# Performance work log

Measured on AMD Instinct MI355X. Metric: run time of the kernel, lower is better.

## Reference

```python
import jax, jax.numpy as jnp
import numpy as np

N_NODES = 100000


def _gcn_layer(h, W, b, src, dst, norm, n):
    # h: [N, Fin] -> transform then normalized scatter-add aggregation
    h = h @ W                                   # [N, Fout]
    msg = h[src] * norm[:, None]                # [E', Fout] gather + scale
    out = jax.ops.segment_sum(msg, dst, num_segments=n)  # scatter-add
    return out + b


def setup_inputs() -> dict:
    key = jax.random.key(0)
    k1, k2, k3, k4 = jax.random.split(key, 4)
    N, F_IN, HID, C, E = N_NODES, 512, 128, 40, 1600000
    x = jax.random.normal(k1, (N, F_IN), dtype=jnp.float32)
    edge_index = jax.random.randint(k2, (2, E), 0, N, dtype=jnp.int64)
    W1 = jax.random.normal(k3, (F_IN, HID), dtype=jnp.float32) * (1.0 / np.sqrt(F_IN))
    b1 = jnp.zeros((HID,), dtype=jnp.float32)
    W2 = jax.random.normal(k4, (HID, C), dtype=jnp.float32) * (1.0 / np.sqrt(HID))
    b2 = jnp.zeros((C,), dtype=jnp.float32)
    return {"x": x, "edge_index": edge_index, "W1": W1, "b1": b1, "W2": W2, "b2": b2}


def reference(x, edge_index, W1, b1, W2, b2):
    n = x.shape[0]
    # add self-loops (GCNConv default)
    loop = jnp.arange(n, dtype=edge_index.dtype)
    src = jnp.concatenate([edge_index[0], loop])
    dst = jnp.concatenate([edge_index[1], loop])
    # symmetric normalization: deg counted on destination (in-degree, incl. self-loop)
    deg = jax.ops.segment_sum(jnp.ones_like(dst, dtype=x.dtype), dst, num_segments=n)
    dis = jnp.where(deg > 0, jax.lax.rsqrt(deg), 0.0)  # deg^{-1/2}
    norm = dis[src] * dis[dst]                          # per-edge weight

    h = jax.nn.relu(_gcn_layer(x, W1, b1, src, dst, norm, n))
    # dropout: identity in eval mode (training=False)
    h = _gcn_layer(h, W2, b2, src, dst, norm, n)
    return jax.nn.log_softmax(h, axis=1)
```

## Files before the change

### kernel.cpp

```cpp
#include <hip/hip_runtime.h>
#include <hip/hip_bf16.h>


#define F_IN 512
#define HID  128
#define NC   40

typedef __attribute__((ext_vector_type(8))) short bf16x8;
typedef __attribute__((ext_vector_type(4))) float f32x4v;

__device__ __forceinline__ ushort f2bf(float f) {
    union { float f; unsigned u; } x; x.f = f;
    unsigned r = x.u + 0x7FFFu + ((x.u >> 16) & 1u);
    return (ushort)(r >> 16);
}
__device__ __forceinline__ float bf2f(ushort u) {
    return __uint_as_float((unsigned)u << 16);
}

__global__ void count_deg(const int* __restrict__ dst, int E, unsigned* __restrict__ cnt) {
    int t = blockIdx.x * blockDim.x + threadIdx.x;
    if (t < E) atomicAdd(&cnt[dst[t]], 1u);
}

__global__ void dis_k(const unsigned* __restrict__ cnt, float* __restrict__ dis, int N) {
    int t = blockIdx.x * blockDim.x + threadIdx.x;
    if (t < N) dis[t] = rsqrtf((float)cnt[t] + 1.0f);
}

__global__ __launch_bounds__(1024) void scan_block(const unsigned* __restrict__ cnt,
                                                   unsigned* __restrict__ offs,
                                                   unsigned* __restrict__ bsums, int N) {
    __shared__ unsigned s[1024];
    int tid = threadIdx.x;
    int i = blockIdx.x * 1024 + tid;
    unsigned v = (i < N) ? cnt[i] + 1u : 0u;
    s[tid] = v;
    __syncthreads();
    #pragma unroll
    for (int d = 1; d < 1024; d <<= 1) {
        unsigned t = (tid >= d) ? s[tid - d] : 0u;
        __syncthreads();
        s[tid] += t;
        __syncthreads();
    }
    if (i < N) offs[i] = s[tid] - v;
    if (tid == 1023) bsums[blockIdx.x] = s[1023];
}

__global__ __launch_bounds__(1024) void scan_bsums(unsigned* __restrict__ bsums, int nb) {
    __shared__ unsigned s[1024];
    int tid = threadIdx.x;
    unsigned v = (tid < nb) ? bsums[tid] : 0u;
    s[tid] = v;
    __syncthreads();
    #pragma unroll
    for (int d = 1; d < 1024; d <<= 1) {
        unsigned t = (tid >= d) ? s[tid - d] : 0u;
        __syncthreads();
        s[tid] += t;
        __syncthreads();
    }
    if (tid < nb) bsums[tid] = s[tid] - v;
}

__global__ __launch_bounds__(1024) void scan_add(unsigned* __restrict__ offs,
                                                 const unsigned* __restrict__ bsums,
                                                 int N, unsigned total) {
    int i = blockIdx.x * 1024 + threadIdx.x;
    if (i < N) offs[i] += bsums[blockIdx.x];
    if (i == 0) offs[N] = total;
}

__global__ void fill_csr(const int* __restrict__ src, const int* __restrict__ dst,
                         const unsigned* __restrict__ offs, unsigned* __restrict__ cursor,
                         int* __restrict__ col, int E, int N) {
    int t = blockIdx.x * blockDim.x + threadIdx.x;
    if (t >= E + N) return;
    int s, d;
    if (t < E) { s = src[t]; d = dst[t]; } else { s = d = t - E; }
    unsigned pos = offs[d] + atomicAdd(&cursor[d], 1u);
    col[pos] = s;
}

__global__ void w1pack(const float* __restrict__ W1, ushort* __restrict__ Bp) {
    int t = blockIdx.x * 256 + threadIdx.x;
    int j = t & 7, n = (t >> 3) & 127, kb = (t >> 10) & 3, s = t >> 12;
    int k = s * 32 + kb * 8 + j;
    Bp[t] = f2bf(W1[(size_t)k * HID + n]);
}

__global__ void w2pack(const float* __restrict__ W2, ushort* __restrict__ Bp) {
    int t = blockIdx.x * 256 + threadIdx.x;
    int j = t & 7;
    int i2 = t >> 3;
    int n = i2 % 48;
    int i3 = i2 / 48;
    int kb = i3 & 3, ks = i3 >> 2;
    int k = ks * 32 + kb * 8 + j;
    float v = (n < NC) ? W2[(size_t)k * NC + n] : 0.f;
    Bp[t] = f2bf(v);
}

__global__ __launch_bounds__(256) void gemm1_mfma(const float* __restrict__ A,
                                                  const ushort* __restrict__ Bp,
                                                  const float* __restrict__ dis,
                                                  ushort* __restrict__ C, int N) {
    __shared__ __align__(16) ushort As[128 * 40];
    __shared__ __align__(16) ushort Bs[4096];
    const int tid  = threadIdx.x;
    const int wave = tid >> 6;
    const int lane = tid & 63;
    const int quad = lane >> 4;
    const int mr   = lane & 15;
    const int bm   = blockIdx.x * 128;

    const int r  = tid >> 1;
    const int hh = tid & 1;
    const bool arow_ok = (bm + r) < N;
    const float* arow = A + (size_t)(bm + r) * F_IN + hh * 16;

    f32x4v acc[2][8];
    #pragma unroll
    for (int i = 0; i < 2; i++)
        #pragma unroll
        for (int t = 0; t < 8; t++)
            acc[i][t] = (f32x4v){0.f, 0.f, 0.f, 0.f};

    for (int s = 0; s < 16; s++) {
        {
            const uint4* srcp = (const uint4*)(Bp + (size_t)s * 4096) + tid * 2;
            uint4 v0 = srcp[0], v1 = srcp[1];
            uint4* dstp = (uint4*)Bs + tid * 2;
            dstp[0] = v0; dstp[1] = v1;
        }
        {
            ushort tmp[16];
            if (arow_ok) {
                const float4* ap = (const float4*)(arow + s * 32);
                #pragma unroll
                for (int i = 0; i < 4; i++) {
                    float4 v = ap[i];
                    tmp[i*4+0] = f2bf(v.x); tmp[i*4+1] = f2bf(v.y);
                    tmp[i*4+2] = f2bf(v.z); tmp[i*4+3] = f2bf(v.w);
                }
            } else {
                #pragma unroll
                for (int i = 0; i < 16; i++) tmp[i] = 0;
            }
            uint4* dstp = (uint4*)&As[r * 40 + hh * 16];
            dstp[0] = ((const uint4*)tmp)[0];
            dstp[1] = ((const uint4*)tmp)[1];
        }
        __syncthreads();
        bf16x8 a0 = *(const bf16x8*)&As[(wave * 32 + mr) * 40 + quad * 8];
        bf16x8 a1 = *(const bf16x8*)&As[(wave * 32 + 16 + mr) * 40 + quad * 8];
        #pragma unroll
        for (int t = 0; t < 8; t++) {
            bf16x8 b = *(const bf16x8*)&Bs[quad * 1024 + (t * 16 + mr) * 8];
            acc[0][t] = __builtin_amdgcn_mfma_f32_16x16x32_bf16(a0, b, acc[0][t], 0, 0, 0);
            acc[1][t] = __builtin_amdgcn_mfma_f32_16x16x32_bf16(a1, b, acc[1][t], 0, 0, 0);
        }
        __syncthreads();
    }
    #pragma unroll
    for (int i = 0; i < 2; i++) {
        int row0 = bm + wave * 32 + i * 16 + quad * 4;
        #pragma unroll
        for (int rr = 0; rr < 4; rr++) {
            int row = row0 + rr;
            if (row < N) {
                float ds = dis[row];
                #pragma unroll
                for (int t = 0; t < 8; t++)
                    C[(size_t)row * HID + t * 16 + mr] = f2bf(acc[i][t][rr] * ds);
            }
        }
    }
}

__global__ __launch_bounds__(256) void agg1_k(const ushort* __restrict__ h,
                                              const int* __restrict__ col,
                                              const unsigned* __restrict__ offs,
                                              const float* __restrict__ dis,
                                              ushort* __restrict__ out, int N) {
    int node = blockIdx.x * 8 + (threadIdx.x >> 5);
    if (node >= N) return;
    int lane = threadIdx.x & 31;
    unsigned p0 = offs[node], p1 = offs[node + 1];
    float4 a0 = make_float4(0.f, 0.f, 0.f, 0.f);
    float4 a1 = make_float4(0.f, 0.f, 0.f, 0.f);
    float4 a2 = make_float4(0.f, 0.f, 0.f, 0.f);
    float4 a3 = make_float4(0.f, 0.f, 0.f, 0.f);
    unsigned p = p0;
    for (; p + 4 <= p1; p += 4) {
        int s0 = col[p], s1 = col[p+1], s2 = col[p+2], s3 = col[p+3];
        ushort4 v0 = *(const ushort4*)(h + (size_t)s0 * HID + lane * 4);
        ushort4 v1 = *(const ushort4*)(h + (size_t)s1 * HID + lane * 4);
        ushort4 v2 = *(const ushort4*)(h + (size_t)s2 * HID + lane * 4);
        ushort4 v3 = *(const ushort4*)(h + (size_t)s3 * HID + lane * 4);
        a0.x += bf2f(v0.x); a0.y += bf2f(v0.y); a0.z += bf2f(v0.z); a0.w += bf2f(v0.w);
        a1.x += bf2f(v1.x); a1.y += bf2f(v1.y); a1.z += bf2f(v1.z); a1.w += bf2f(v1.w);
        a2.x += bf2f(v2.x); a2.y += bf2f(v2.y); a2.z += bf2f(v2.z); a2.w += bf2f(v2.w);
        a3.x += bf2f(v3.x); a3.y += bf2f(v3.y); a3.z += bf2f(v3.z); a3.w += bf2f(v3.w);
    }
    for (; p < p1; ++p) {
        int s = col[p];
        ushort4 v = *(const ushort4*)(h + (size_t)s * HID + lane * 4);
        a0.x += bf2f(v.x); a0.y += bf2f(v.y); a0.z += bf2f(v.z); a0.w += bf2f(v.w);
    }
    float dd = dis[node];
    float4 a;
    a.x = ((a0.x + a1.x) + (a2.x + a3.x)) * dd;
    a.y = ((a0.y + a1.y) + (a2.y + a3.y)) * dd;
    a.z = ((a0.z + a1.z) + (a2.z + a3.z)) * dd;
    a.w = ((a0.w + a1.w) + (a2.w + a3.w)) * dd;
    ushort4 o;
    o.x = f2bf(a.x); o.y = f2bf(a.y); o.z = f2bf(a.z); o.w = f2bf(a.w);
    *(ushort4*)(out + (size_t)node * HID + lane * 4) = o;
}

__global__ __launch_bounds__(256) void gemm2_mfma(const ushort* __restrict__ A,
                                                  const float* __restrict__ b1,
                                                  const ushort* __restrict__ W2p,
                                                  const float* __restrict__ dis,
                                                  ushort* __restrict__ h2, int N) {
    __shared__ __align__(16) ushort As[128 * 136];
    __shared__ __align__(16) ushort Bs[6144];
    const int tid = threadIdx.x;
    const int bm = blockIdx.x * 128;

    {
        const uint4* s4 = (const uint4*)W2p;
        uint4* d4 = (uint4*)Bs;
        #pragma unroll
        for (int i = 0; i < 3; i++) d4[tid + i * 256] = s4[tid + i * 256];
    }
    {
        const int r  = tid >> 1;
        const int hh = tid & 1;
        const int row = bm + r;
        const float* brow = b1 + hh * 64;
        if (row < N) {
            const ushort* arow = A + (size_t)row * HID + hh * 64;
            #pragma unroll
            for (int i = 0; i < 8; i++) {
                uint4 raw = *(const uint4*)(arow + i * 8);
                const ushort* u = (const ushort*)&raw;
                ushort tmp[8];
                #pragma unroll
                for (int j = 0; j < 8; j++)
                    tmp[j] = f2bf(fmaxf(bf2f(u[j]) + brow[i * 8 + j], 0.f));
                *(uint4*)&As[r * 136 + hh * 64 + i * 8] = *(const uint4*)tmp;
            }
        } else {
            #pragma unroll
            for (int i = 0; i < 8; i++) {
                uint4 z = {0, 0, 0, 0};
                *(uint4*)&As[r * 136 + hh * 64 + i * 8] = z;
            }
        }
    }
    __syncthreads();

    const int wave = tid >> 6;
    const int lane = tid & 63;
    const int quad = lane >> 4;
    const int mr   = lane & 15;
    f32x4v acc[2][3];
    #pragma unroll
    for (int i = 0; i < 2; i++)
        #pragma unroll
        for (int t = 0; t < 3; t++)
            acc[i][t] = (f32x4v){0.f, 0.f, 0.f, 0.f};
    #pragma unroll
    for (int ks = 0; ks < 4; ks++) {
        bf16x8 a0 = *(const bf16x8*)&As[(wave * 32 + mr) * 136 + ks * 32 + quad * 8];
        bf16x8 a1 = *(const bf16x8*)&As[(wave * 32 + 16 + mr) * 136 + ks * 32 + quad * 8];
        #pragma unroll
        for (int t = 0; t < 3; t++) {
            bf16x8 b = *(const bf16x8*)&Bs[((ks * 4 + quad) * 48 + t * 16 + mr) * 8];
            acc[0][t] = __builtin_amdgcn_mfma_f32_16x16x32_bf16(a0, b, acc[0][t], 0, 0, 0);
            acc[1][t] = __builtin_amdgcn_mfma_f32_16x16x32_bf16(a1, b, acc[1][t], 0, 0, 0);
        }
    }
    #pragma unroll
    for (int i = 0; i < 2; i++) {
        #pragma unroll
        for (int rr = 0; rr < 4; rr++) {
            int node = bm + wave * 32 + i * 16 + quad * 4 + rr;
            if (node < N) {
                float ds = dis[node];
                #pragma unroll
                for (int t = 0; t < 3; t++) {
                    int c = t * 16 + mr;
                    if (c < NC)
                        h2[(size_t)node * NC + c] = f2bf(acc[i][t][rr] * ds);
                }
            }
        }
    }
}

__global__ __launch_bounds__(256) void agg2_ls(const ushort* __restrict__ h2,
                                               const int* __restrict__ col,
                                               const unsigned* __restrict__ offs,
                                               const float* __restrict__ dis,
                                               const float* __restrict__ b2,
                                               float* __restrict__ out, int N) {
    int node = blockIdx.x * 32 + (threadIdx.x >> 3);
    if (node >= N) return;
    int lane = threadIdx.x & 7;
    unsigned p0 = offs[node], p1 = offs[node + 1];
    float4 a  = make_float4(0.f, 0.f, 0.f, 0.f);
    float4 a2 = make_float4(0.f, 0.f, 0.f, 0.f);
    float4 c  = make_float4(0.f, 0.f, 0.f, 0.f);
    float4 c2 = make_float4(0.f, 0.f, 0.f, 0.f);
    unsigned p = p0;
    for (; p + 2 <= p1; p += 2) {
        int s0 = col[p], s1 = col[p + 1];
        const ushort* hp0 = h2 + (size_t)s0 * NC;
        const ushort* hp1 = h2 + (size_t)s1 * NC;
        ushort4 v0 = *(const ushort4*)(hp0 + lane * 4);
        ushort4 v1 = *(const ushort4*)(hp1 + lane * 4);
        a.x += bf2f(v0.x); a.y += bf2f(v0.y); a.z += bf2f(v0.z); a.w += bf2f(v0.w);
        c.x += bf2f(v1.x); c.y += bf2f(v1.y); c.z += bf2f(v1.z); c.w += bf2f(v1.w);
        if (lane < 2) {
            ushort4 w0 = *(const ushort4*)(hp0 + 32 + lane * 4);
            ushort4 w1 = *(const ushort4*)(hp1 + 32 + lane * 4);
            a2.x += bf2f(w0.x); a2.y += bf2f(w0.y); a2.z += bf2f(w0.z); a2.w += bf2f(w0.w);
            c2.x += bf2f(w1.x); c2.y += bf2f(w1.y); c2.z += bf2f(w1.z); c2.w += bf2f(w1.w);
        }
    }
    for (; p < p1; ++p) {
        int s = col[p];
        const ushort* hp = h2 + (size_t)s * NC;
        ushort4 v = *(const ushort4*)(hp + lane * 4);
        a.x += bf2f(v.x); a.y += bf2f(v.y); a.z += bf2f(v.z); a.w += bf2f(v.w);
        if (lane < 2) {
            ushort4 w = *(const ushort4*)(hp + 32 + lane * 4);
            a2.x += bf2f(w.x); a2.y += bf2f(w.y); a2.z += bf2f(w.z); a2.w += bf2f(w.w);
        }
    }
    float dd = dis[node];
    float4 bb = *(const float4*)(b2 + lane * 4);
    a.x = (a.x + c.x) * dd + bb.x; a.y = (a.y + c.y) * dd + bb.y;
    a.z = (a.z + c.z) * dd + bb.z; a.w = (a.w + c.w) * dd + bb.w;
    if (lane < 2) {
        float4 b2v = *(const float4*)(b2 + 32 + lane * 4);
        a2.x = (a2.x + c2.x) * dd + b2v.x; a2.y = (a2.y + c2.y) * dd + b2v.y;
        a2.z = (a2.z + c2.z) * dd + b2v.z; a2.w = (a2.w + c2.w) * dd + b2v.w;
    }
    float m = fmaxf(fmaxf(a.x, a.y), fmaxf(a.z, a.w));
    if (lane < 2) m = fmaxf(m, fmaxf(fmaxf(a2.x, a2.y), fmaxf(a2.z, a2.w)));
    #pragma unroll
    for (int d = 1; d < 8; d <<= 1) m = fmaxf(m, __shfl_xor(m, d, 8));
    float s = __expf(a.x - m) + __expf(a.y - m) + __expf(a.z - m) + __expf(a.w - m);
    if (lane < 2) s += __expf(a2.x - m) + __expf(a2.y - m) + __expf(a2.z - m) + __expf(a2.w - m);
    #pragma unroll
    for (int d = 1; d < 8; d <<= 1) s += __shfl_xor(s, d, 8);
    float lse = m + __logf(s);
    float* op = out + (size_t)node * NC;
    *(float4*)(op + lane * 4) = make_float4(a.x - lse, a.y - lse, a.z - lse, a.w - lse);
    if (lane < 2)
        *(float4*)(op + 32 + lane * 4) = make_float4(a2.x - lse, a2.y - lse, a2.z - lse, a2.w - lse);
}

extern "C" void kernel_launch(void* const* d_in, const int* in_sizes, int n_in,
                              void* d_out, int out_size, void* d_ws, size_t ws_size,
                              hipStream_t stream) {
    const float* x  = (const float*)d_in[0];
    const int*   ei = (const int*)d_in[1];
    const float* W1 = (const float*)d_in[2];
    const float* b1 = (const float*)d_in[3];
    const float* W2 = (const float*)d_in[4];
    const float* b2 = (const float*)d_in[5];
    float* out = (float*)d_out;

    const int N = in_sizes[0] / F_IN;
    const int E = in_sizes[1] / 2;
    const int EN = E + N;
    const int* src = ei;
    const int* dst = ei + E;

    char* ws = (char*)d_ws;
    size_t o = 0;
    unsigned* cnt  = (unsigned*)(ws + o); o += (size_t)N * 4;
    float*    dis  = (float*)   (ws + o); o += (size_t)N * 4;
    unsigned* offs = (unsigned*)(ws + o); o += (size_t)(N + 4) * 4;
    unsigned* bsums= (unsigned*)(ws + o); o += 4096;
    int*      col  = (int*)     (ws + o); o += (size_t)EN * 4;
    o = (o + 15) & ~(size_t)15;
    ushort*   W1p  = (ushort*)  (ws + o); o += (size_t)F_IN * HID * 2;
    o = (o + 15) & ~(size_t)15;
    ushort*   W2p  = (ushort*)  (ws + o); o += 6144 * 2;
    o = (o + 15) & ~(size_t)15;
    ushort*   h1   = (ushort*)  (ws + o); o += (size_t)N * HID * 2;
    o = (o + 15) & ~(size_t)15;
    ushort*   ag1  = (ushort*)  (ws + o); o += (size_t)N * HID * 2;
    o = (o + 15) & ~(size_t)15;
    ushort*   h2   = (ushort*)  (ws + o); o += (size_t)N * NC * 2;

    const int nb = (N + 1023) / 1024;

    hipMemsetAsync(cnt, 0, (size_t)N * 4, stream);
    count_deg<<<(E + 255) / 256, 256, 0, stream>>>(dst, E, cnt);
    dis_k<<<(N + 255) / 256, 256, 0, stream>>>(cnt, dis, N);

    scan_block<<<nb, 1024, 0, stream>>>(cnt, offs, bsums, N);
    scan_bsums<<<1, 1024, 0, stream>>>(bsums, nb);
    scan_add<<<nb, 1024, 0, stream>>>(offs, bsums, N, (unsigned)EN);

    hipMemsetAsync(cnt, 0, (size_t)N * 4, stream);
    fill_csr<<<(EN + 255) / 256, 256, 0, stream>>>(src, dst, offs, cnt, col, E, N);

    w1pack<<<(F_IN * HID) / 256, 256, 0, stream>>>(W1, W1p);
    w2pack<<<6144 / 256, 256, 0, stream>>>(W2, W2p);

    gemm1_mfma<<<(N + 127) / 128, 256, 0, stream>>>(x, W1p, dis, h1, N);
    agg1_k<<<(N + 7) / 8, 256, 0, stream>>>(h1, col, offs, dis, ag1, N);

    gemm2_mfma<<<(N + 127) / 128, 256, 0, stream>>>(ag1, b1, W2p, dis, h2, N);
    agg2_ls<<<(N + 31) / 32, 256, 0, stream>>>(h2, col, offs, dis, b2, out, N);
}
```

Measured before the change: 618.6 us.

## Fuse setup kernels, drop self-loop CSR entries, double-buffer gemm1, widen aggregation loads

Moves the deg^-1/2 computation into the scan kernel and merges the two weight-pack kernels into one launch. Self-loops are no longer stored in the CSR; each aggregation instead reads the node's own row directly, which shrinks the edge list and drops the second memset. gemm1 now loads A fragments straight from global memory into registers and double-buffers the B tile in shared memory, removing the A staging through shared memory. Both aggregation kernels switch to 16-byte loads per lane, with fewer lanes per node and idle lanes in agg2 for the 40-class case.

```diff
diff --git a/kernel.cpp b/kernel.cpp
--- a/kernel.cpp
+++ b/kernel.cpp
@@ -23,18 +23,15 @@
     if (t < E) atomicAdd(&cnt[dst[t]], 1u);
 }
 
-__global__ void dis_k(const unsigned* __restrict__ cnt, float* __restrict__ dis, int N) {
-    int t = blockIdx.x * blockDim.x + threadIdx.x;
-    if (t < N) dis[t] = rsqrtf((float)cnt[t] + 1.0f);
-}
-
 __global__ __launch_bounds__(1024) void scan_block(const unsigned* __restrict__ cnt,
                                                    unsigned* __restrict__ offs,
-                                                   unsigned* __restrict__ bsums, int N) {
+                                                   unsigned* __restrict__ bsums,
+                                                   float* __restrict__ dis, int N) {
     __shared__ unsigned s[1024];
     int tid = threadIdx.x;
     int i = blockIdx.x * 1024 + tid;
-    unsigned v = (i < N) ? cnt[i] + 1u : 0u;
+    unsigned v = (i < N) ? cnt[i] : 0u;
+    if (i < N) dis[i] = rsqrtf((float)v + 1.0f);
     s[tid] = v;
     __syncthreads();
     #pragma unroll
@@ -74,40 +71,41 @@
 
 __global__ void fill_csr(const int* __restrict__ src, const int* __restrict__ dst,
                          const unsigned* __restrict__ offs, unsigned* __restrict__ cursor,
-                         int* __restrict__ col, int E, int N) {
+                         int* __restrict__ col, int E) {
     int t = blockIdx.x * blockDim.x + threadIdx.x;
-    if (t >= E + N) return;
-    int s, d;
-    if (t < E) { s = src[t]; d = dst[t]; } else { s = d = t - E; }
+    if (t >= E) return;
+    int s = src[t], d = dst[t];
     unsigned pos = offs[d] + atomicAdd(&cursor[d], 1u);
     col[pos] = s;
 }
 
-__global__ void w1pack(const float* __restrict__ W1, ushort* __restrict__ Bp) {
+__global__ void packW(const float* __restrict__ W1, const float* __restrict__ W2,
+                      ushort* __restrict__ W1p, ushort* __restrict__ W2p) {
     int t = blockIdx.x * 256 + threadIdx.x;
-    int j = t & 7, n = (t >> 3) & 127, kb = (t >> 10) & 3, s = t >> 12;
-    int k = s * 32 + kb * 8 + j;
-    Bp[t] = f2bf(W1[(size_t)k * HID + n]);
-}
-
-__global__ void w2pack(const float* __restrict__ W2, ushort* __restrict__ Bp) {
-    int t = blockIdx.x * 256 + threadIdx.x;
-    int j = t & 7;
-    int i2 = t >> 3;
-    int n = i2 % 48;
-    int i3 = i2 / 48;
-    int kb = i3 & 3, ks = i3 >> 2;
-    int k = ks * 32 + kb * 8 + j;
-    float v = (n < NC) ? W2[(size_t)k * NC + n] : 0.f;
-    Bp[t] = f2bf(v);
+    if (t < 65536) {
+        int j = t & 7, n = (t >> 3) & 127, kb = (t >> 10) & 3, s = t >> 12;
+        int k = s * 32 + kb * 8 + j;
+        W1p[t] = f2bf(W1[(size_t)k * HID + n]);
+    } else {
+        int q = t - 65536;
+        if (q < 6144) {
+            int j = q & 7;
+            int i2 = q >> 3;
+            int n = i2 % 48;
+            int i3 = i2 / 48;
+            int kb = i3 & 3, ks = i3 >> 2;
+            int k = ks * 32 + kb * 8 + j;
+            float v = (n < NC) ? W2[(size_t)k * NC + n] : 0.f;
+            W2p[q] = f2bf(v);
+        }
+    }
 }
 
 __global__ __launch_bounds__(256) void gemm1_mfma(const float* __restrict__ A,
                                                   const ushort* __restrict__ Bp,
                                                   const float* __restrict__ dis,
                                                   ushort* __restrict__ C, int N) {
-    __shared__ __align__(16) ushort As[128 * 40];
-    __shared__ __align__(16) ushort Bs[4096];
+    __shared__ __align__(16) ushort Bs[2][4096];
     const int tid  = threadIdx.x;
     const int wave = tid >> 6;
     const int lane = tid & 63;
@@ -115,10 +113,11 @@
     const int mr   = lane & 15;
     const int bm   = blockIdx.x * 128;
 
-    const int r  = tid >> 1;
-    const int hh = tid & 1;
-    const bool arow_ok = (bm + r) < N;
-    const float* arow = A + (size_t)(bm + r) * F_IN + hh * 16;
+    const int r0 = bm + wave * 32 + mr;
+    const int r1 = r0 + 16;
+    const bool ok0 = r0 < N, ok1 = r1 < N;
+    const float* arow0 = A + (size_t)r0 * F_IN + quad * 8;
+    const float* arow1 = A + (size_t)r1 * F_IN + quad * 8;
 
     f32x4v acc[2][8];
     #pragma unroll
@@ -127,39 +126,39 @@
         for (int t = 0; t < 8; t++)
             acc[i][t] = (f32x4v){0.f, 0.f, 0.f, 0.f};
 
+    {
+        const uint4* sp = (const uint4*)Bp;
+        uint4* dp = (uint4*)Bs[0];
+        dp[tid] = sp[tid];
+        dp[tid + 256] = sp[tid + 256];
+    }
+    __syncthreads();
+
     for (int s = 0; s < 16; s++) {
-        {
-            const uint4* srcp = (const uint4*)(Bp + (size_t)s * 4096) + tid * 2;
-            uint4 v0 = srcp[0], v1 = srcp[1];
-            uint4* dstp = (uint4*)Bs + tid * 2;
-            dstp[0] = v0; dstp[1] = v1;
-        }
-        {
-            ushort tmp[16];
-            if (arow_ok) {
-                const float4* ap = (const float4*)(arow + s * 32);
-                #pragma unroll
-                for (int i = 0; i < 4; i++) {
-                    float4 v = ap[i];
-                    tmp[i*4+0] = f2bf(v.x); tmp[i*4+1] = f2bf(v.y);
-                    tmp[i*4+2] = f2bf(v.z); tmp[i*4+3] = f2bf(v.w);
-                }
-            } else {
-                #pragma unroll
-                for (int i = 0; i < 16; i++) tmp[i] = 0;
-            }
-            uint4* dstp = (uint4*)&As[r * 40 + hh * 16];
-            dstp[0] = ((const uint4*)tmp)[0];
-            dstp[1] = ((const uint4*)tmp)[1];
-        }
-        __syncthreads();
-        bf16x8 a0 = *(const bf16x8*)&As[(wave * 32 + mr) * 40 + quad * 8];
-        bf16x8 a1 = *(const bf16x8*)&As[(wave * 32 + 16 + mr) * 40 + quad * 8];
+        if (s < 15) {
+            const uint4* sp = (const uint4*)(Bp + (size_t)(s + 1) * 4096);
+            uint4* dp = (uint4*)Bs[(s + 1) & 1];
+            dp[tid] = sp[tid];
+            dp[tid + 256] = sp[tid + 256];
+        }
+        float4 z = make_float4(0.f, 0.f, 0.f, 0.f);
+        float4 a0l = ok0 ? *(const float4*)(arow0 + s * 32)     : z;
+        float4 a0h = ok0 ? *(const float4*)(arow0 + s * 32 + 4) : z;
+        float4 a1l = ok1 ? *(const float4*)(arow1 + s * 32)     : z;
+        float4 a1h = ok1 ? *(const float4*)(arow1 + s * 32 + 4) : z;
+        __align__(16) ushort ta[8], tb[8];
+        ta[0]=f2bf(a0l.x); ta[1]=f2bf(a0l.y); ta[2]=f2bf(a0l.z); ta[3]=f2bf(a0l.w);
+        ta[4]=f2bf(a0h.x); ta[5]=f2bf(a0h.y); ta[6]=f2bf(a0h.z); ta[7]=f2bf(a0h.w);
+        tb[0]=f2bf(a1l.x); tb[1]=f2bf(a1l.y); tb[2]=f2bf(a1l.z); tb[3]=f2bf(a1l.w);
+        tb[4]=f2bf(a1h.x); tb[5]=f2bf(a1h.y); tb[6]=f2bf(a1h.z); tb[7]=f2bf(a1h.w);
+        bf16x8 fa0 = *(const bf16x8*)ta;
+        bf16x8 fa1 = *(const bf16x8*)tb;
+        const ushort* bbase = Bs[s & 1] + quad * 1024;
         #pragma unroll
         for (int t = 0; t < 8; t++) {
-            bf16x8 b = *(const bf16x8*)&Bs[quad * 1024 + (t * 16 + mr) * 8];
-            acc[0][t] = __builtin_amdgcn_mfma_f32_16x16x32_bf16(a0, b, acc[0][t], 0, 0, 0);
-            acc[1][t] = __builtin_amdgcn_mfma_f32_16x16x32_bf16(a1, b, acc[1][t], 0, 0, 0);
+            bf16x8 b = *(const bf16x8*)&bbase[(t * 16 + mr) * 8];
+            acc[0][t] = __builtin_amdgcn_mfma_f32_16x16x32_bf16(fa0, b, acc[0][t], 0, 0, 0);
+            acc[1][t] = __builtin_amdgcn_mfma_f32_16x16x32_bf16(fa1, b, acc[1][t], 0, 0, 0);
         }
         __syncthreads();
     }
@@ -184,40 +183,48 @@
                                               const unsigned* __restrict__ offs,
                                               const float* __restrict__ dis,
                                               ushort* __restrict__ out, int N) {
-    int node = blockIdx.x * 8 + (threadIdx.x >> 5);
+    int node = blockIdx.x * 16 + (threadIdx.x >> 4);
     if (node >= N) return;
-    int lane = threadIdx.x & 31;
+    int lane = threadIdx.x & 15;
+    const size_t coff = (size_t)lane * 8;
+    float a0[8], a1[8] = {}, a2[8] = {}, a3[8] = {};
+    {
+        uint4 v = *(const uint4*)(h + (size_t)node * HID + coff);
+        const ushort* u = (const ushort*)&v;
+        #pragma unroll
+        for (int j = 0; j < 8; j++) a0[j] = bf2f(u[j]);
+    }
     unsigned p0 = offs[node], p1 = offs[node + 1];
-    float4 a0 = make_float4(0.f, 0.f, 0.f, 0.f);
-    float4 a1 = make_float4(0.f, 0.f, 0.f, 0.f);
-    float4 a2 = make_float4(0.f, 0.f, 0.f, 0.f);
-    float4 a3 = make_float4(0.f, 0.f, 0.f, 0.f);
     unsigned p = p0;
     for (; p + 4 <= p1; p += 4) {
         int s0 = col[p], s1 = col[p+1], s2 = col[p+2], s3 = col[p+3];
-        ushort4 v0 = *(const ushort4*)(h + (size_t)s0 * HID + lane * 4);
-        ushort4 v1 = *(const ushort4*)(h + (size_t)s1 * HID + lane * 4);
-        ushort4 v2 = *(const ushort4*)(h + (size_t)s2 * HID + lane * 4);
-        ushort4 v3 = *(const ushort4*)(h + (size_t)s3 * HID + lane * 4);
-        a0.x += bf2f(v0.x); a0.y += bf2f(v0.y); a0.z += bf2f(v0.z); a0.w += bf2f(v0.w);
-        a1.x += bf2f(v1.x); a1.y += bf2f(v1.y); a1.z += bf2f(v1.z); a1.w += bf2f(v1.w);
-        a2.x += bf2f(v2.x); a2.y += bf2f(v2.y); a2.z += bf2f(v2.z); a2.w += bf2f(v2.w);
-        a3.x += bf2f(v3.x); a3.y += bf2f(v3.y); a3.z += bf2f(v3.z); a3.w += bf2f(v3.w);
+        uint4 v0 = *(const uint4*)(h + (size_t)s0 * HID + coff);
+        uint4 v1 = *(const uint4*)(h + (size_t)s1 * HID + coff);
+        uint4 v2 = *(const uint4*)(h + (size_t)s2 * HID + coff);
+        uint4 v3 = *(const uint4*)(h + (size_t)s3 * HID + coff);
+        const ushort* u0 = (const ushort*)&v0;
+        const ushort* u1 = (const ushort*)&v1;
+        const ushort* u2 = (const ushort*)&v2;
+        const ushort* u3 = (const ushort*)&v3;
+        #pragma unroll
+        for (int j = 0; j < 8; j++) {
+            a0[j] += bf2f(u0[j]); a1[j] += bf2f(u1[j]);
+            a2[j] += bf2f(u2[j]); a3[j] += bf2f(u3[j]);
+        }
     }
     for (; p < p1; ++p) {
         int s = col[p];
-        ushort4 v = *(const ushort4*)(h + (size_t)s * HID + lane * 4);
-        a0.x += bf2f(v.x); a0.y += bf2f(v.y); a0.z += bf2f(v.z); a0.w += bf2f(v.w);
+        uint4 v = *(const uint4*)(h + (size_t)s * HID + coff);
+        const ushort* u = (const ushort*)&v;
+        #pragma unroll
+        for (int j = 0; j < 8; j++) a0[j] += bf2f(u[j]);
     }
     float dd = dis[node];
-    float4 a;
-    a.x = ((a0.x + a1.x) + (a2.x + a3.x)) * dd;
-    a.y = ((a0.y + a1.y) + (a2.y + a3.y)) * dd;
-    a.z = ((a0.z + a1.z) + (a2.z + a3.z)) * dd;
-    a.w = ((a0.w + a1.w) + (a2.w + a3.w)) * dd;
-    ushort4 o;
-    o.x = f2bf(a.x); o.y = f2bf(a.y); o.z = f2bf(a.z); o.w = f2bf(a.w);
-    *(ushort4*)(out + (size_t)node * HID + lane * 4) = o;
+    __align__(16) ushort o[8];
+    #pragma unroll
+    for (int j = 0; j < 8; j++)
+        o[j] = f2bf(((a0[j] + a1[j]) + (a2[j] + a3[j])) * dd);
+    *(uint4*)(out + (size_t)node * HID + coff) = *(const uint4*)o;
 }
 
 __global__ __launch_bounds__(256) void gemm2_mfma(const ushort* __restrict__ A,
@@ -247,7 +254,7 @@
             for (int i = 0; i < 8; i++) {
                 uint4 raw = *(const uint4*)(arow + i * 8);
                 const ushort* u = (const ushort*)&raw;
-                ushort tmp[8];
+                __align__(16) ushort tmp[8];
                 #pragma unroll
                 for (int j = 0; j < 8; j++)
                     tmp[j] = f2bf(fmaxf(bf2f(u[j]) + brow[i * 8 + j], 0.f));
@@ -256,8 +263,8 @@
         } else {
             #pragma unroll
             for (int i = 0; i < 8; i++) {
-                uint4 z = {0, 0, 0, 0};
-                *(uint4*)&As[r * 136 + hh * 64 + i * 8] = z;
+                uint4 zz = {0, 0, 0, 0};
+                *(uint4*)&As[r * 136 + hh * 64 + i * 8] = zz;
             }
         }
     }
@@ -311,59 +318,62 @@
     int node = blockIdx.x * 32 + (threadIdx.x >> 3);
     if (node >= N) return;
     int lane = threadIdx.x & 7;
+    const bool act = lane < 5;
+    const size_t coff = (size_t)lane * 8;
+    float a[8] = {}, c[8] = {};
+    if (act) {
+        uint4 v = *(const uint4*)(h2 + (size_t)node * NC + coff);
+        const ushort* u = (const ushort*)&v;
+        #pragma unroll
+        for (int j = 0; j < 8; j++) a[j] = bf2f(u[j]);
+    }
     unsigned p0 = offs[node], p1 = offs[node + 1];
-    float4 a  = make_float4(0.f, 0.f, 0.f, 0.f);
-    float4 a2 = make_float4(0.f, 0.f, 0.f, 0.f);
-    float4 c  = make_float4(0.f, 0.f, 0.f, 0.f);
-    float4 c2 = make_float4(0.f, 0.f, 0.f, 0.f);
     unsigned p = p0;
     for (; p + 2 <= p1; p += 2) {
         int s0 = col[p], s1 = col[p + 1];
-        const ushort* hp0 = h2 + (size_t)s0 * NC;
-        const ushort* hp1 = h2 + (size_t)s1 * NC;
-        ushort4 v0 = *(const ushort4*)(hp0 + lane * 4);
-        ushort4 v1 = *(const ushort4*)(hp1 + lane * 4);
-        a.x += bf2f(v0.x); a.y += bf2f(v0.y); a.z += bf2f(v0.z); a.w += bf2f(v0.w);
-        c.x += bf2f(v1.x); c.y += bf2f(v1.y); c.z += bf2f(v1.z); c.w += bf2f(v1.w);
-        if (lane < 2) {
-            ushort4 w0 = *(const ushort4*)(hp0 + 32 + lane * 4);
-            ushort4 w1 = *(const ushort4*)(hp1 + 32 + lane * 4);
-            a2.x += bf2f(w0.x); a2.y += bf2f(w0.y); a2.z += bf2f(w0.z); a2.w += bf2f(w0.w);
-            c2.x += bf2f(w1.x); c2.y += bf2f(w1.y); c2.z += bf2f(w1.z); c2.w += bf2f(w1.w);
+        if (act) {
+            uint4 v0 = *(const uint4*)(h2 + (size_t)s0 * NC + coff);
+            uint4 v1 = *(const uint4*)(h2 + (size_t)s1 * NC + coff);
+            const ushort* u0 = (const ushort*)&v0;
+            const ushort* u1 = (const ushort*)&v1;
+            #pragma unroll
+            for (int j = 0; j < 8; j++) { a[j] += bf2f(u0[j]); c[j] += bf2f(u1[j]); }
         }
     }
     for (; p < p1; ++p) {
         int s = col[p];
-        const ushort* hp = h2 + (size_t)s * NC;
-        ushort4 v = *(const ushort4*)(hp + lane * 4);
-        a.x += bf2f(v.x); a.y += bf2f(v.y); a.z += bf2f(v.z); a.w += bf2f(v.w);
-        if (lane < 2) {
-            ushort4 w = *(const ushort4*)(hp + 32 + lane * 4);
-            a2.x += bf2f(w.x); a2.y += bf2f(w.y); a2.z += bf2f(w.z); a2.w += bf2f(w.w);
+        if (act) {
+            uint4 v = *(const uint4*)(h2 + (size_t)s * NC + coff);
+            const ushort* u = (const ushort*)&v;
+            #pragma unroll
+            for (int j = 0; j < 8; j++) a[j] += bf2f(u[j]);
         }
     }
     float dd = dis[node];
-    float4 bb = *(const float4*)(b2 + lane * 4);
-    a.x = (a.x + c.x) * dd + bb.x; a.y = (a.y + c.y) * dd + bb.y;
-    a.z = (a.z + c.z) * dd + bb.z; a.w = (a.w + c.w) * dd + bb.w;
-    if (lane < 2) {
-        float4 b2v = *(const float4*)(b2 + 32 + lane * 4);
-        a2.x = (a2.x + c2.x) * dd + b2v.x; a2.y = (a2.y + c2.y) * dd + b2v.y;
-        a2.z = (a2.z + c2.z) * dd + b2v.z; a2.w = (a2.w + c2.w) * dd + b2v.w;
-    }
-    float m = fmaxf(fmaxf(a.x, a.y), fmaxf(a.z, a.w));
-    if (lane < 2) m = fmaxf(m, fmaxf(fmaxf(a2.x, a2.y), fmaxf(a2.z, a2.w)));
+    float l[8];
+    float m = -1e30f;
+    if (act) {
+        #pragma unroll
+        for (int j = 0; j < 8; j++) {
+            l[j] = (a[j] + c[j]) * dd + b2[lane * 8 + j];
+            m = fmaxf(m, l[j]);
+        }
+    }
     #pragma unroll
     for (int d = 1; d < 8; d <<= 1) m = fmaxf(m, __shfl_xor(m, d, 8));
-    float s = __expf(a.x - m) + __expf(a.y - m) + __expf(a.z - m) + __expf(a.w - m);
-    if (lane < 2) s += __expf(a2.x - m) + __expf(a2.y - m) + __expf(a2.z - m) + __expf(a2.w - m);
+    float s = 0.f;
+    if (act) {
+        #pragma unroll
+        for (int j = 0; j < 8; j++) s += __expf(l[j] - m);
+    }
     #pragma unroll
     for (int d = 1; d < 8; d <<= 1) s += __shfl_xor(s, d, 8);
     float lse = m + __logf(s);
-    float* op = out + (size_t)node * NC;
-    *(float4*)(op + lane * 4) = make_float4(a.x - lse, a.y - lse, a.z - lse, a.w - lse);
-    if (lane < 2)
-        *(float4*)(op + 32 + lane * 4) = make_float4(a2.x - lse, a2.y - lse, a2.z - lse, a2.w - lse);
+    if (act) {
+        float* op = out + (size_t)node * NC + lane * 8;
+        *(float4*)op       = make_float4(l[0]-lse, l[1]-lse, l[2]-lse, l[3]-lse);
+        *(float4*)(op + 4) = make_float4(l[4]-lse, l[5]-lse, l[6]-lse, l[7]-lse);
+    }
 }
 
 extern "C" void kernel_launch(void* const* d_in, const int* in_sizes, int n_in,
@@ -379,17 +389,17 @@
 
     const int N = in_sizes[0] / F_IN;
     const int E = in_sizes[1] / 2;
-    const int EN = E + N;
     const int* src = ei;
     const int* dst = ei + E;
 
     char* ws = (char*)d_ws;
     size_t o = 0;
     unsigned* cnt  = (unsigned*)(ws + o); o += (size_t)N * 4;
+    unsigned* cur  = (unsigned*)(ws + o); o += (size_t)N * 4;
     float*    dis  = (float*)   (ws + o); o += (size_t)N * 4;
     unsigned* offs = (unsigned*)(ws + o); o += (size_t)(N + 4) * 4;
     unsigned* bsums= (unsigned*)(ws + o); o += 4096;
-    int*      col  = (int*)     (ws + o); o += (size_t)EN * 4;
+    int*      col  = (int*)     (ws + o); o += (size_t)E * 4;
     o = (o + 15) & ~(size_t)15;
     ushort*   W1p  = (ushort*)  (ws + o); o += (size_t)F_IN * HID * 2;
     o = (o + 15) & ~(size_t)15;
@@ -403,22 +413,17 @@
 
     const int nb = (N + 1023) / 1024;
 
-    hipMemsetAsync(cnt, 0, (size_t)N * 4, stream);
+    hipMemsetAsync(cnt, 0, (size_t)N * 8, stream);
     count_deg<<<(E + 255) / 256, 256, 0, stream>>>(dst, E, cnt);
-    dis_k<<<(N + 255) / 256, 256, 0, stream>>>(cnt, dis, N);
-
-    scan_block<<<nb, 1024, 0, stream>>>(cnt, offs, bsums, N);
+    scan_block<<<nb, 1024, 0, stream>>>(cnt, offs, bsums, dis, N);
     scan_bsums<<<1, 1024, 0, stream>>>(bsums, nb);
-    scan_add<<<nb, 1024, 0, stream>>>(offs, bsums, N, (unsigned)EN);
-
-    hipMemsetAsync(cnt, 0, (size_t)N * 4, stream);
-    fill_csr<<<(EN + 255) / 256, 256, 0, stream>>>(src, dst, offs, cnt, col, E, N);
-
-    w1pack<<<(F_IN * HID) / 256, 256, 0, stream>>>(W1, W1p);
-    w2pack<<<6144 / 256, 256, 0, stream>>>(W2, W2p);
+    scan_add<<<nb, 1024, 0, stream>>>(offs, bsums, N, (unsigned)E);
+    fill_csr<<<(E + 255) / 256, 256, 0, stream>>>(src, dst, offs, cur, col, E);
+
+    packW<<<(65536 + 6144 + 255) / 256, 256, 0, stream>>>(W1, W2, W1p, W2p);
 
     gemm1_mfma<<<(N + 127) / 128, 256, 0, stream>>>(x, W1p, dis, h1, N);
-    agg1_k<<<(N + 7) / 8, 256, 0, stream>>>(h1, col, offs, dis, ag1, N);
+    agg1_k<<<(N + 15) / 16, 256, 0, stream>>>(h1, col, offs, dis, ag1, N);
 
     gemm2_mfma<<<(N + 127) / 128, 256, 0, stream>>>(ag1, b1, W2p, dis, h2, N);
     agg2_ls<<<(N + 31) / 32, 256, 0, stream>>>(h2, col, offs, dis, b2, out, N);
```

New measurement: 661.0 us. 6.9% more time.
